# Optimization experiments

Measured on AMD Instinct MI355X. Metric: run time of the kernel, lower is better.

The kernel has to match this reference:

```python
import jax, jax.numpy as jnp
import numpy as np
import math

B, S, D = 2, 2048, 2048
H, KVH, WIN = 16, 4, 256
HD = D // H            # 128
QPER = H // KVH        # 4


def setup_inputs() -> dict:
    key = jax.random.key(0)
    ks = jax.random.split(key, 9)
    s = lambda k, shp: jax.random.normal(k, shp, dtype=jnp.float32) * 0.02
    return {
        "x": jax.random.normal(ks[0], (B, S, D), dtype=jnp.float32),
        "Wq": s(ks[1], (D, D)),            "bq": jnp.zeros((D,), jnp.float32),
        "Wk": s(ks[2], (D, KVH * HD)),      "bk": jnp.zeros((KVH * HD,), jnp.float32),
        "Wv": s(ks[3], (D, KVH * HD)),      "bv": jnp.zeros((KVH * HD,), jnp.float32),
        "Wo": s(ks[4], (D, D)),            "bo": jnp.zeros((D,), jnp.float32),
    }


def reference(x, Wq, bq, Wk, bk, Wv, bv, Wo, bo):
    b, s, _ = x.shape
    # projections
    Q = (x @ Wq + bq).reshape(b, s, H, HD).transpose(0, 2, 1, 3)     # [b,H,s,hd]
    K = (x @ Wk + bk).reshape(b, s, KVH, HD).transpose(0, 2, 1, 3)   # [b,kvh,s,hd]
    V = (x @ Wv + bv).reshape(b, s, KVH, HD).transpose(0, 2, 1, 3)   # [b,kvh,s,hd]
    # GQA grouping: head h = g*QPER + q
    Qg = Q.reshape(b, KVH, QPER, s, HD)                               # [b,g,q,s,hd]
    scores = jnp.einsum('bgqsd,bgtd->bgqst', Qg, K)                   # [b,g,q,s,s]
    i = jnp.arange(s)[:, None]
    j = jnp.arange(s)[None, :]
    keep = (j <= i) & (j >= i - WIN + 1)                              # [s,s]
    scores = jnp.where(keep, scores, -jnp.inf)
    A = jax.nn.softmax(scores / math.sqrt(HD), axis=-1)
    O = jnp.einsum('bgqst,bgtd->bgqsd', A, V)                         # [b,g,q,s,hd]
    O = O.reshape(b, H, s, HD).transpose(0, 2, 1, 3).reshape(b, s, D)
    return O @ Wo + bo
```

## Files before the change

kernel.cpp:

```cpp
#include <hip/hip_runtime.h>
#include <hip/hip_bf16.h>
#include <math.h>

typedef __bf16 bf16_t;
typedef bf16_t bf16x8 __attribute__((ext_vector_type(8)));
typedef bf16_t bf16x4 __attribute__((ext_vector_type(4)));
typedef float  f32x4  __attribute__((ext_vector_type(4)));

#define NB    2
#define SEQ   2048
#define DIM   2048
#define NHEAD 16
#define NKVH  4
#define HDIM  128
#define WINSZ 256
#define KVD   512
#define QKVN  3072
#define MROWS 4096

__device__ __forceinline__ void async_copy16(const void* g, void* lds) {
    __builtin_amdgcn_global_load_lds(
        (const __attribute__((address_space(1))) void*)g,
        (__attribute__((address_space(3))) void*)lds,
        16, 0, 0);
}

__global__ __launch_bounds__(256) void preprocess(
    const float* __restrict__ x,  const float* __restrict__ Wq,
    const float* __restrict__ bq, const float* __restrict__ Wk,
    const float* __restrict__ bk, const float* __restrict__ Wv,
    const float* __restrict__ bv, const float* __restrict__ Wo,
    bf16_t* __restrict__ xb, bf16_t* __restrict__ WqkvT,
    bf16_t* __restrict__ WoT, float* __restrict__ bqkv) {
    __shared__ float tile[32][33];
    const int tid = threadIdx.x;
    int bid = blockIdx.x;
    if (bid < 8192) {
        int i = (bid * 256 + tid) * 4;
        float4 v = *(const float4*)(x + i);
        bf16x4 o;
        o[0] = (bf16_t)v.x; o[1] = (bf16_t)v.y; o[2] = (bf16_t)v.z; o[3] = (bf16_t)v.w;
        *(bf16x4*)(xb + i) = o;
        return;
    }
    bid -= 8192;
    const float* src; bf16_t* dst; int N;
    if (bid < 4096)       { src = Wq; dst = WqkvT;                          N = DIM; }
    else if (bid < 5120)  { src = Wk; dst = WqkvT + (size_t)DIM * DIM;      N = KVD; bid -= 4096; }
    else if (bid < 6144)  { src = Wv; dst = WqkvT + (size_t)(DIM+KVD)*DIM;  N = KVD; bid -= 5120; }
    else if (bid < 10240) { src = Wo; dst = WoT;                            N = DIM; bid -= 6144; }
    else {
        int i = (bid - 10240) * 256 + tid;
        if (i < QKVN) {
            float v = (i < DIM) ? bq[i] : ((i < DIM + KVD) ? bk[i - DIM] : bv[i - DIM - KVD]);
            bqkv[i] = v;
        }
        return;
    }
    const int K = DIM;
    int ntile = N / 32;
    int n0 = (bid % ntile) * 32, k0 = (bid / ntile) * 32;
    int tx = tid & 31, ty = tid >> 5;
    for (int r = ty; r < 32; r += 8)
        tile[r][tx] = src[(size_t)(k0 + r) * N + n0 + tx];
    __syncthreads();
    for (int r = ty; r < 32; r += 8)
        dst[(size_t)(n0 + r) * K + k0 + tx] = (bf16_t)tile[tx][r];
}

template <int BM, int BN, typename OutT, bool VFUSE>
__global__ __launch_bounds__(512, 1) void gemm8p(const bf16_t* __restrict__ A,
                                                 const bf16_t* __restrict__ Bt,
                                                 const float* __restrict__ bias,
                                                 OutT* __restrict__ C,
                                                 bf16_t* __restrict__ vtb,
                                                 int M, int N, int K, float qs, int qcols) {
    constexpr int ASLOTS = BM / 16;
    constexpr int BSLOTS = BN / 16;
    constexpr int MF   = BM / 32;
    constexpr int NF   = BN / 64;
    constexpr int AHALF = BM * 32;
    constexpr int BHALF = BN * 32;
    constexpr int BUFSZ = 2 * (AHALF + BHALF);
    __shared__ bf16_t lds[2 * BUFSZ];

    const int tid  = threadIdx.x;
    const int wave = tid >> 6;
    const int lane = tid & 63;
    const int lg = lane >> 4, lc = lane & 15;
    const int wr = wave >> 2, wc = wave & 3;

    const int nbn  = N / BN;
    const int nblk = (M / BM) * nbn;
    const int qq   = nblk >> 3;
    const int swz  = (blockIdx.x & 7) * qq + (blockIdx.x >> 3);
    const long brow = (long)(swz / nbn) * BM;
    const long bcol = (long)(swz % nbn) * BN;

    const int aiss = (ASLOTS - wave + 7) >> 3;
    const int biss = (BSLOTS - wave + 7) >> 3;
    const int miss = aiss + biss;

    f32x4 acc[MF][NF] = {};

    auto stage = [&](int buf, int p, int kt) {
        const int kcol = kt * 64 + p * 32;
        const int srow = lane >> 2;
        const int sch  = lane & 3;
        {
            bf16_t* d = lds + buf * BUFSZ + p * AHALF;
#pragma unroll
            for (int s = wave; s < ASLOTS; s += 8) {
                int row = s * 16 + srow;
                int ch  = sch ^ ((row >> 1) & 3);
                async_copy16(A + (brow + row) * (long)K + kcol + ch * 8, d + s * 512);
            }
        }
        {
            bf16_t* d = lds + buf * BUFSZ + 2 * AHALF + p * BHALF;
#pragma unroll
            for (int s = wave; s < BSLOTS; s += 8) {
                int row = s * 16 + srow;
                int ch  = sch ^ ((row >> 1) & 3);
                async_copy16(Bt + (bcol + row) * (long)K + kcol + ch * 8, d + s * 512);
            }
        }
    };

    stage(0, 0, 0);
    stage(0, 1, 0);

    const int NT = K >> 6;
    const int cswz = (lg ^ ((lc >> 1) & 3)) * 8;
    for (int t = 0; t < NT; ++t) {
#pragma unroll
        for (int p = 0; p < 2; ++p) {
            if (t == NT - 1 && p == 1) {
                asm volatile("s_waitcnt vmcnt(0)" ::: "memory");
            } else if (miss == 4) {
                asm volatile("s_waitcnt vmcnt(4)" ::: "memory");
            } else if (miss == 3) {
                asm volatile("s_waitcnt vmcnt(3)" ::: "memory");
            } else {
                asm volatile("s_waitcnt vmcnt(2)" ::: "memory");
            }
            __builtin_amdgcn_s_barrier();
            asm volatile("" ::: "memory");
            const bf16_t* Ab = lds + (t & 1) * BUFSZ + p * AHALF;
            const bf16_t* Bb = lds + (t & 1) * BUFSZ + 2 * AHALF + p * BHALF;
            bf16x8 af[MF], bv[NF];
#pragma unroll
            for (int m = 0; m < MF; ++m)
                af[m] = *(const bf16x8*)(Ab + (wr * (BM / 2) + m * 16 + lc) * 32 + cswz);
#pragma unroll
            for (int n = 0; n < NF; ++n)
                bv[n] = *(const bf16x8*)(Bb + (wc * (BN / 4) + n * 16 + lc) * 32 + cswz);
            if (t + 1 < NT) stage((t + 1) & 1, p, t + 1);
            __builtin_amdgcn_s_setprio(1);
#pragma unroll
            for (int m = 0; m < MF; ++m)
#pragma unroll
                for (int n = 0; n < NF; ++n)
                    acc[m][n] = __builtin_amdgcn_mfma_f32_16x16x32_bf16(af[m], bv[n], acc[m][n], 0, 0, 0);
            __builtin_amdgcn_s_setprio(0);
        }
    }

#pragma unroll
    for (int n = 0; n < NF; ++n) {
        int gc = (int)bcol + wc * (BN / 4) + n * 16 + lc;
        float bvs = bias[gc];
        if constexpr (VFUSE) {
            if (gc >= DIM + KVD) {
                int vg = (gc - (DIM + KVD)) >> 7;
                int dl = (gc - (DIM + KVD)) & 127;
#pragma unroll
                for (int m = 0; m < MF; ++m) {
                    long gr = brow + wr * (BM / 2) + m * 16 + 4 * lg;
                    int bb = (int)(gr >> 11);
                    int js = (int)(gr & (SEQ - 1));
                    bf16x4 ov;
#pragma unroll
                    for (int r = 0; r < 4; ++r) ov[r] = (bf16_t)(acc[m][n][r] + bvs);
                    *(bf16x4*)(vtb + (((size_t)(bb * NKVH) + vg) * 64 + (js >> 5)) * 4096
                                   + dl * 32 + (js & 31)) = ov;
                }
                continue;
            }
        }
        bool ds = gc < qcols;
#pragma unroll
        for (int m = 0; m < MF; ++m) {
            long gr = brow + wr * (BM / 2) + m * 16 + 4 * lg;
#pragma unroll
            for (int r = 0; r < 4; ++r) {
                float v = acc[m][n][r] + bvs;
                if (ds) v *= qs;
                C[(gr + r) * (long)N + gc] = (OutT)v;
            }
        }
    }
}

__global__ __launch_bounds__(256) void attn_kernel(const bf16_t* __restrict__ QKV,
                                                   const bf16_t* __restrict__ Vtb,
                                                   bf16_t* __restrict__ Ob) {
    __shared__ bf16_t Kls[3][32 * 128];
    __shared__ bf16_t Vls[3][128 * 32];
    __shared__ bf16_t Pls[4][32 * 40];

    const int wv   = threadIdx.x >> 6;
    const int lane = threadIdx.x & 63;
    const int lg = lane >> 4, lc = lane & 15;

    const int swb = (blockIdx.x & 7) * 64 + (blockIdx.x >> 3);
    const int ti = swb & 63;
    const int g  = (swb >> 6) & 3;
    const int b  = swb >> 8;
    const int h  = g * 4 + wv;
    const int i0 = ti * 32;
    bf16_t* P = &Pls[wv][0];

    bf16x8 qf[2][4];
#pragma unroll
    for (int sq = 0; sq < 2; ++sq) {
        const bf16_t* qp = QKV + ((size_t)(b * SEQ) + i0 + sq * 16 + lc) * QKVN + h * HDIM + lg * 8;
#pragma unroll
        for (int kk = 0; kk < 4; ++kk) qf[sq][kk] = *(const bf16x8*)(qp + kk * 32);
    }

    auto stage = [&](int buf, int jb) {
        const int j0s = jb * 32;
        const bf16_t* kgb = QKV + ((size_t)(b * SEQ) + j0s) * QKVN + DIM + g * HDIM;
#pragma unroll
        for (int ii = 0; ii < 2; ++ii) {
            int i = wv * 2 + ii;
            int row = i * 4 + (lane >> 4);
            int ch  = (lane & 15) ^ (row & 7);
            async_copy16(kgb + (size_t)row * QKVN + ch * 8, &Kls[buf][i * 512]);
        }
        const bf16_t* vgb = Vtb + (((size_t)(b * NKVH) + g) * 64 + jb) * 4096;
#pragma unroll
        for (int ii = 0; ii < 2; ++ii) {
            int i = wv * 2 + ii;
            int row = i * 16 + (lane >> 2);
            int ch  = (lane & 3) ^ ((row ^ (row >> 2)) & 3);
            async_copy16(vgb + row * 32 + ch * 8, &Vls[buf][i * 512]);
        }
    };

    float m_run[2] = {-1e30f, -1e30f}, l_run[2] = {0.f, 0.f};
    f32x4 oacc[2][8] = {};

    int jlo = i0 - (WINSZ - 1); if (jlo < 0) jlo = 0;
    const int jb0 = jlo >> 5;
    const int jb1 = (i0 + 31) >> 5;

    stage(0, jb0);
    if (jb0 + 1 <= jb1) stage(1, jb0 + 1);

    for (int jb = jb0; jb <= jb1; ++jb) {
        const int j0 = jb * 32;
        const int it = jb - jb0;
        const int cur = it % 3;
        if (jb < jb1) asm volatile("s_waitcnt vmcnt(4)" ::: "memory");
        else          asm volatile("s_waitcnt vmcnt(0)" ::: "memory");
        __builtin_amdgcn_s_barrier();
        asm volatile("" ::: "memory");

        bf16x8 kf[2][4];
#pragma unroll
        for (int t = 0; t < 2; ++t)
#pragma unroll
            for (int kk = 0; kk < 4; ++kk) {
                int row = t * 16 + lc;
                int ch  = (kk * 4 + lg) ^ (row & 7);
                kf[t][kk] = *(const bf16x8*)(&Kls[cur][row * 128 + ch * 8]);
            }
        if (jb + 2 <= jb1) stage((it + 2) % 3, jb + 2);
        asm volatile("s_waitcnt lgkmcnt(0)" ::: "memory");
        __builtin_amdgcn_sched_barrier(0);

        f32x4 s[2][2];
        __builtin_amdgcn_s_setprio(1);
#pragma unroll
        for (int t = 0; t < 2; ++t)
#pragma unroll
            for (int sq = 0; sq < 2; ++sq) {
                f32x4 sv = {};
#pragma unroll
                for (int kk = 0; kk < 4; ++kk)
                    sv = __builtin_amdgcn_mfma_f32_16x16x32_bf16(kf[t][kk], qf[sq][kk], sv, 0, 0, 0);
                s[t][sq] = sv;
            }
        __builtin_amdgcn_s_setprio(0);

        const bool edge = (j0 < i0 - (WINSZ - 32)) || (j0 > i0 - 31);
        if (edge) {
#pragma unroll
            for (int t = 0; t < 2; ++t)
#pragma unroll
                for (int sq = 0; sq < 2; ++sq) {
                    int irow = i0 + sq * 16 + lc;
#pragma unroll
                    for (int r = 0; r < 4; ++r) {
                        int j = j0 + t * 16 + 4 * lg + r;
                        if (j > irow || j < irow - (WINSZ - 1)) s[t][sq][r] = -1e30f;
                    }
                }
        }
        float tmax[2];
#pragma unroll
        for (int sq = 0; sq < 2; ++sq) {
            float tm = fmaxf(fmaxf(fmaxf(s[0][sq][0], s[0][sq][1]), fmaxf(s[0][sq][2], s[0][sq][3])),
                             fmaxf(fmaxf(s[1][sq][0], s[1][sq][1]), fmaxf(s[1][sq][2], s[1][sq][3])));
            tm = fmaxf(tm, __shfl_xor(tm, 16, 64));
            tm = fmaxf(tm, __shfl_xor(tm, 32, 64));
            tmax[sq] = tm;
        }
        if (!__all(tmax[0] - m_run[0] <= 8.0f && tmax[1] - m_run[1] <= 8.0f)) {
#pragma unroll
            for (int sq = 0; sq < 2; ++sq) {
                float m_new = fmaxf(m_run[sq], tmax[sq]);
                float resc = __builtin_amdgcn_exp2f(m_run[sq] - m_new);
                l_run[sq] *= resc;
#pragma unroll
                for (int c = 0; c < 8; ++c) {
                    oacc[sq][c][0] *= resc; oacc[sq][c][1] *= resc;
                    oacc[sq][c][2] *= resc; oacc[sq][c][3] *= resc;
                }
                m_run[sq] = m_new;
            }
        }
        float psum[2] = {0.f, 0.f};
#pragma unroll
        for (int t = 0; t < 2; ++t)
#pragma unroll
            for (int sq = 0; sq < 2; ++sq) {
                bf16x4 pk;
#pragma unroll
                for (int r = 0; r < 4; ++r) {
                    float sv = s[t][sq][r];
                    float p = (edge && sv < -5e29f) ? 0.f : __builtin_amdgcn_exp2f(sv - m_run[sq]);
                    psum[sq] += p;
                    pk[r] = (bf16_t)p;
                }
                *(bf16x4*)(P + (sq * 16 + lc) * 40 + t * 16 + lg * 4) = pk;
            }
#pragma unroll
        for (int sq = 0; sq < 2; ++sq) {
            float ps = psum[sq];
            ps += __shfl_xor(ps, 16, 64);
            ps += __shfl_xor(ps, 32, 64);
            l_run[sq] += ps;
        }
        asm volatile("" ::: "memory");

        bf16x8 vf[8];
#pragma unroll
        for (int c = 0; c < 8; ++c) {
            int row = c * 16 + lc;
            int ch  = lg ^ ((row ^ (row >> 2)) & 3);
            vf[c] = *(const bf16x8*)(&Vls[cur][row * 32 + ch * 8]);
        }
        bf16x8 pf[2];
#pragma unroll
        for (int sq = 0; sq < 2; ++sq)
            pf[sq] = *(const bf16x8*)(P + (sq * 16 + lc) * 40 + lg * 8);

        __builtin_amdgcn_s_setprio(1);
#pragma unroll
        for (int c = 0; c < 8; ++c)
#pragma unroll
            for (int sq = 0; sq < 2; ++sq)
                oacc[sq][c] = __builtin_amdgcn_mfma_f32_16x16x32_bf16(vf[c], pf[sq], oacc[sq][c], 0, 0, 0);
        __builtin_amdgcn_s_setprio(0);
    }

#pragma unroll
    for (int sq = 0; sq < 2; ++sq) {
        const float inv = 1.f / l_run[sq];
#pragma unroll
        for (int c = 0; c < 8; ++c) {
            bf16x4 ov;
#pragma unroll
            for (int r = 0; r < 4; ++r) ov[r] = (bf16_t)(oacc[sq][c][r] * inv);
            *(bf16x4*)(Ob + ((size_t)(b * SEQ) + i0 + sq * 16 + lc) * DIM + h * HDIM + c * 16 + lg * 4) = ov;
        }
    }
}

extern "C" void kernel_launch(void* const* d_in, const int* in_sizes, int n_in,
                              void* d_out, int out_size, void* d_ws, size_t ws_size,
                              hipStream_t stream) {
    const float* x  = (const float*)d_in[0];
    const float* Wq = (const float*)d_in[1];
    const float* bq = (const float*)d_in[2];
    const float* Wk = (const float*)d_in[3];
    const float* bk = (const float*)d_in[4];
    const float* Wv = (const float*)d_in[5];
    const float* bv = (const float*)d_in[6];
    const float* Wo = (const float*)d_in[7];
    const float* bo = (const float*)d_in[8];
    float* out = (float*)d_out;

    char* ws = (char*)d_ws;
    bf16_t* xb    = (bf16_t*)(ws);
    bf16_t* WqkvT = (bf16_t*)(ws + (16u << 20));
    bf16_t* WoT   = (bf16_t*)(ws + (28u << 20));
    bf16_t* QKVb  = (bf16_t*)(ws + (36u << 20));
    float*  bqkv  = (float*) (ws + (60u << 20));
    bf16_t* Vtb   = (bf16_t*)(ws + (61u << 20));
    bf16_t* Ob    = xb;

    const float qs = 0.12751707498038074f;

    preprocess<<<18444, 256, 0, stream>>>(x, Wq, bq, Wk, bk, Wv, bv, Wo,
                                          xb, WqkvT, WoT, bqkv);

    gemm8p<256, 192, bf16_t, true><<<dim3((MROWS / 256) * (QKVN / 192)), 512, 0, stream>>>(
        xb, WqkvT, bqkv, QKVb, Vtb, MROWS, QKVN, DIM, qs, DIM);

    attn_kernel<<<dim3(NB * NKVH * (SEQ / 32)), 256, 0, stream>>>(QKVb, Vtb, Ob);

    gemm8p<128, 256, float, false><<<dim3((MROWS / 128) * (DIM / 256)), 512, 0, stream>>>(
        Ob, WoT, bo, out, nullptr, MROWS, DIM, DIM, 1.0f, 0);
}
```

Before: 143.2 us.

## Use one barrier per K-tile and configurable wave grid in GEMM

Replaces the per-half-tile partial vmcnt waits and barriers with a single full vmcnt(0) wait and barrier per 64-wide K step. It drops the s_setprio hints and makes the wave layout a template parameter, using a 4x2 wave grid for the QKV GEMM (was 2x4) and keeping 2x4 for the output projection. Fewer barriers cut sync overhead, but the full vmcnt(0) wait stops the next stage's loads from overlapping the current compute. The new grid also changes per-wave fragment counts and LDS reads.

After: 144.1 us. About the same (+0.6%).

```diff
diff --git a/kernel.cpp b/kernel.cpp
--- a/kernel.cpp
+++ b/kernel.cpp
@@ -68,17 +68,18 @@
         dst[(size_t)(n0 + r) * K + k0 + tx] = (bf16_t)tile[tx][r];
 }
 
-template <int BM, int BN, typename OutT, bool VFUSE>
-__global__ __launch_bounds__(512, 1) void gemm8p(const bf16_t* __restrict__ A,
+template <int BM, int BN, int MPOS, typename OutT, bool VFUSE>
+__global__ __launch_bounds__(512, 1) void gemm1b(const bf16_t* __restrict__ A,
                                                  const bf16_t* __restrict__ Bt,
                                                  const float* __restrict__ bias,
                                                  OutT* __restrict__ C,
                                                  bf16_t* __restrict__ vtb,
                                                  int M, int N, int K, float qs, int qcols) {
+    constexpr int NPOS = 8 / MPOS;
     constexpr int ASLOTS = BM / 16;
     constexpr int BSLOTS = BN / 16;
-    constexpr int MF   = BM / 32;
-    constexpr int NF   = BN / 64;
+    constexpr int MF = BM / MPOS / 16;
+    constexpr int NF = BN / NPOS / 16;
     constexpr int AHALF = BM * 32;
     constexpr int BHALF = BN * 32;
     constexpr int BUFSZ = 2 * (AHALF + BHALF);
@@ -88,7 +89,7 @@
     const int wave = tid >> 6;
     const int lane = tid & 63;
     const int lg = lane >> 4, lc = lane & 15;
-    const int wr = wave >> 2, wc = wave & 3;
+    const int wr = wave / NPOS, wc = wave % NPOS;
 
     const int nbn  = N / BN;
     const int nblk = (M / BM) * nbn;
@@ -97,10 +98,6 @@
     const long brow = (long)(swz / nbn) * BM;
     const long bcol = (long)(swz % nbn) * BN;
 
-    const int aiss = (ASLOTS - wave + 7) >> 3;
-    const int biss = (BSLOTS - wave + 7) >> 3;
-    const int miss = aiss + biss;
-
     f32x4 acc[MF][NF] = {};
 
     auto stage = [&](int buf, int p, int kt) {
@@ -133,42 +130,33 @@
     const int NT = K >> 6;
     const int cswz = (lg ^ ((lc >> 1) & 3)) * 8;
     for (int t = 0; t < NT; ++t) {
+        asm volatile("s_waitcnt vmcnt(0)" ::: "memory");
+        __builtin_amdgcn_s_barrier();
+        asm volatile("" ::: "memory");
+        const bf16_t* base = lds + (t & 1) * BUFSZ;
 #pragma unroll
         for (int p = 0; p < 2; ++p) {
-            if (t == NT - 1 && p == 1) {
-                asm volatile("s_waitcnt vmcnt(0)" ::: "memory");
-            } else if (miss == 4) {
-                asm volatile("s_waitcnt vmcnt(4)" ::: "memory");
-            } else if (miss == 3) {
-                asm volatile("s_waitcnt vmcnt(3)" ::: "memory");
-            } else {
-                asm volatile("s_waitcnt vmcnt(2)" ::: "memory");
-            }
-            __builtin_amdgcn_s_barrier();
-            asm volatile("" ::: "memory");
-            const bf16_t* Ab = lds + (t & 1) * BUFSZ + p * AHALF;
-            const bf16_t* Bb = lds + (t & 1) * BUFSZ + 2 * AHALF + p * BHALF;
+            const bf16_t* Ab = base + p * AHALF;
+            const bf16_t* Bb = base + 2 * AHALF + p * BHALF;
             bf16x8 af[MF], bv[NF];
 #pragma unroll
             for (int m = 0; m < MF; ++m)
-                af[m] = *(const bf16x8*)(Ab + (wr * (BM / 2) + m * 16 + lc) * 32 + cswz);
+                af[m] = *(const bf16x8*)(Ab + (wr * (BM / MPOS) + m * 16 + lc) * 32 + cswz);
 #pragma unroll
             for (int n = 0; n < NF; ++n)
-                bv[n] = *(const bf16x8*)(Bb + (wc * (BN / 4) + n * 16 + lc) * 32 + cswz);
+                bv[n] = *(const bf16x8*)(Bb + (wc * (BN / NPOS) + n * 16 + lc) * 32 + cswz);
             if (t + 1 < NT) stage((t + 1) & 1, p, t + 1);
-            __builtin_amdgcn_s_setprio(1);
 #pragma unroll
             for (int m = 0; m < MF; ++m)
 #pragma unroll
                 for (int n = 0; n < NF; ++n)
                     acc[m][n] = __builtin_amdgcn_mfma_f32_16x16x32_bf16(af[m], bv[n], acc[m][n], 0, 0, 0);
-            __builtin_amdgcn_s_setprio(0);
         }
     }
 
 #pragma unroll
     for (int n = 0; n < NF; ++n) {
-        int gc = (int)bcol + wc * (BN / 4) + n * 16 + lc;
+        int gc = (int)bcol + wc * (BN / NPOS) + n * 16 + lc;
         float bvs = bias[gc];
         if constexpr (VFUSE) {
             if (gc >= DIM + KVD) {
@@ -176,7 +164,7 @@
                 int dl = (gc - (DIM + KVD)) & 127;
 #pragma unroll
                 for (int m = 0; m < MF; ++m) {
-                    long gr = brow + wr * (BM / 2) + m * 16 + 4 * lg;
+                    long gr = brow + wr * (BM / MPOS) + m * 16 + 4 * lg;
                     int bb = (int)(gr >> 11);
                     int js = (int)(gr & (SEQ - 1));
                     bf16x4 ov;
@@ -191,7 +179,7 @@
         bool ds = gc < qcols;
 #pragma unroll
         for (int m = 0; m < MF; ++m) {
-            long gr = brow + wr * (BM / 2) + m * 16 + 4 * lg;
+            long gr = brow + wr * (BM / MPOS) + m * 16 + 4 * lg;
 #pragma unroll
             for (int r = 0; r < 4; ++r) {
                 float v = acc[m][n][r] + bvs;
@@ -418,11 +406,11 @@
     preprocess<<<18444, 256, 0, stream>>>(x, Wq, bq, Wk, bk, Wv, bv, Wo,
                                           xb, WqkvT, WoT, bqkv);
 
-    gemm8p<256, 192, bf16_t, true><<<dim3((MROWS / 256) * (QKVN / 192)), 512, 0, stream>>>(
+    gemm1b<256, 192, 4, bf16_t, true><<<dim3((MROWS / 256) * (QKVN / 192)), 512, 0, stream>>>(
         xb, WqkvT, bqkv, QKVb, Vtb, MROWS, QKVN, DIM, qs, DIM);
 
     attn_kernel<<<dim3(NB * NKVH * (SEQ / 32)), 256, 0, stream>>>(QKVb, Vtb, Ob);
 
-    gemm8p<128, 256, float, false><<<dim3((MROWS / 128) * (DIM / 256)), 512, 0, stream>>>(
+    gemm1b<128, 256, 2, float, false><<<dim3((MROWS / 128) * (DIM / 256)), 512, 0, stream>>>(
         Ob, WoT, bo, out, nullptr, MROWS, DIM, DIM, 1.0f, 0);
 }
```
